# Kernel tuning notes

Measured on AMD Instinct MI355X. Metric: run time of the kernel, lower is better.

Reference implementation:

```python
import jax, jax.numpy as jnp
import numpy as np

COST_CLASS = 1.0
COST_REG = 1.0
NUM_TGT = 5  # targets per batch element, implied by `sizes = [5] * ...`

# All 5^5 = 3125 ways for each of the 5 targets to pick one of its 5 cheapest queries.
_CHOICES = np.stack(np.meshgrid(*([np.arange(NUM_TGT)] * NUM_TGT), indexing='ij'), -1).reshape(-1, NUM_TGT)


def _solve_lap5(cost):
    """Exact rectangular linear_sum_assignment for cost [num_queries, 5].

    Exchange argument: some optimal matching assigns every target (column) to one of
    its 5 cheapest queries (at most 4 of them can be taken by the other targets).
    So enumerate 5^5 candidate tuples, mask duplicates, take the argmin.
    Returns (row_ind, col_ind) sorted by row like scipy.linear_sum_assignment.
    """
    neg_vals, idx = jax.lax.top_k(-cost.T, NUM_TGT)          # [5 targets, 5 candidates]
    vals = -neg_vals
    choices = jnp.asarray(_CHOICES)                          # [3125, 5]
    t = jnp.arange(NUM_TGT)
    cand_q = idx[t[None, :], choices]                        # [3125, 5] query index per target
    cand_c = vals[t[None, :], choices]                       # [3125, 5] matching cost per target
    sq = jnp.sort(cand_q, axis=-1)
    valid = jnp.all(sq[:, 1:] != sq[:, :-1], axis=-1)        # all chosen queries distinct
    total = jnp.where(valid, cand_c.sum(-1), jnp.inf)
    best = jnp.argmin(total)
    rows = cand_q[best]                                      # [5] query index per target 0..4
    order = jnp.argsort(rows)
    return rows[order].astype(jnp.int32), order.astype(jnp.int32)


def setup_inputs() -> dict:
    key = jax.random.key(0)
    k1, k2, k3, k4 = jax.random.split(key, 4)
    bs, nq, T = 32, 2048, 32 * NUM_TGT
    return {
        'pred_logits': jax.random.normal(k1, (bs, nq, 1), dtype=jnp.float32),
        'pred_regs': jax.random.normal(k2, (bs, nq, 3), dtype=jnp.float32),
        'labels': jax.random.randint(k3, (T,), 0, 2, dtype=jnp.int32),
        'tgt_regression': jax.random.normal(k4, (T, 3), dtype=jnp.float32),
    }


def reference(pred_logits, pred_regs, labels, tgt_regression):
    bs, nq = pred_logits.shape[:2]
    # out_prob = softmax(pred_logits) is computed in the original but never used
    # (and tgt labels are unused): classification cost reduces to the constant cost_class.
    out_bbox = pred_regs.reshape(bs * nq, 3)
    # L1 cdist against ALL targets, as in the original: [bs*nq, T]
    cost_reg = jnp.sum(jnp.abs(out_bbox[:, None, :] - tgt_regression[None, :, :]), axis=-1)
    C = COST_REG * cost_reg + COST_CLASS
    # split the target axis into per-batch blocks of 5 and keep the diagonal block
    C = C.reshape(bs, nq, bs, NUM_TGT)
    b = jnp.arange(bs)
    Cb = C[b, :, b, :]                                       # [bs, nq, 5]
    rows, cols = jax.vmap(_solve_lap5)(Cb)                   # each [bs, 5]
    return rows, cols
```

## Files before the change

kernel.cpp:

```cpp
#include <hip/hip_runtime.h>

#define NUM_TGT 5

__device__ __forceinline__ bool lex_less(float c1, int q1, float c2, int q2) {
    return (c1 < c2) || (c1 == c2 && q1 < q2);
}

__device__ __forceinline__ void insert5(float c[5], int q[5], float cv, int qv) {
    if (lex_less(cv, qv, c[4], q[4])) {
        c[4] = cv; q[4] = qv;
#pragma unroll
        for (int i = 3; i >= 0; --i) {
            if (lex_less(c[i + 1], q[i + 1], c[i], q[i])) {
                float tc = c[i]; c[i] = c[i + 1]; c[i + 1] = tc;
                int   tq = q[i]; q[i] = q[i + 1]; q[i + 1] = tq;
            }
        }
    }
}

__global__ __launch_bounds__(256)
void topk_kernel(const float* __restrict__ pred_regs,
                 const float* __restrict__ tgt_reg,
                 float* __restrict__ ws_c,
                 int* __restrict__ ws_q,
                 int nq) {
    const int bt   = blockIdx.x;
    const int b    = bt / NUM_TGT;
    const int tid  = threadIdx.x;
    const int wave = tid >> 6;
    const int lane = tid & 63;

    __shared__ float wc[4][NUM_TGT];
    __shared__ int   wq[4][NUM_TGT];

    const float t0 = tgt_reg[bt * 3 + 0];
    const float t1 = tgt_reg[bt * 3 + 1];
    const float t2 = tgt_reg[bt * 3 + 2];

    float c[5] = {INFINITY, INFINITY, INFINITY, INFINITY, INFINITY};
    int   q[5] = {0x7fffffff, 0x7fffffff, 0x7fffffff, 0x7fffffff, 0x7fffffff};

    const float* base = pred_regs + (size_t)b * nq * 3;
#pragma unroll
    for (int j = 0; j < 8; ++j) {
        const int qi = j * 256 + tid;
        if (qi < nq) {
            float cost = fabsf(base[qi * 3 + 0] - t0);
            cost = cost + fabsf(base[qi * 3 + 1] - t1);
            cost = cost + fabsf(base[qi * 3 + 2] - t2);
            cost = cost + 1.0f;
            insert5(c, q, cost, qi);
        }
    }

#pragma unroll
    for (int m = 1; m < 64; m <<= 1) {
#pragma unroll
        for (int i = 0; i < 5; ++i) {
            float oc = __shfl_xor(c[i], m, 64);
            int   oq = __shfl_xor(q[i], m, 64);
            insert5(c, q, oc, oq);
        }
    }

    if (lane == 0) {
#pragma unroll
        for (int i = 0; i < 5; ++i) { wc[wave][i] = c[i]; wq[wave][i] = q[i]; }
    }
    __syncthreads();

    if (tid == 0) {
#pragma unroll
        for (int w = 1; w < 4; ++w)
#pragma unroll
            for (int i = 0; i < 5; ++i)
                insert5(c, q, wc[w][i], wq[w][i]);
#pragma unroll
        for (int i = 0; i < 5; ++i) {
            ws_c[bt * NUM_TGT + i] = c[i];
            ws_q[bt * NUM_TGT + i] = q[i];
        }
    }
}

__global__ __launch_bounds__(256)
void enumerate_kernel(const float* __restrict__ ws_c,
                      const int* __restrict__ ws_q,
                      int* __restrict__ out,
                      int bs) {
    const int b    = blockIdx.x;
    const int tid  = threadIdx.x;
    const int wave = tid >> 6;
    const int lane = tid & 63;

    __shared__ float top_c[NUM_TGT][NUM_TGT];
    __shared__ int   top_q[NUM_TGT][NUM_TGT];
    __shared__ float red_t[4];
    __shared__ int   red_k[4];

    if (tid < 25) {
        top_c[tid / 5][tid % 5] = ws_c[b * 25 + tid];
        top_q[tid / 5][tid % 5] = ws_q[b * 25 + tid];
    }
    __syncthreads();

    float bt = INFINITY;
    int   bk = 0x7fffffff;
    for (int k = tid; k < 3125; k += 256) {
        int r  = k;
        const int d0 = r / 625; r -= d0 * 625;
        const int d1 = r / 125; r -= d1 * 125;
        const int d2 = r / 25;  r -= d2 * 25;
        const int d3 = r / 5;
        const int d4 = r - d3 * 5;

        const int q0 = top_q[0][d0], q1 = top_q[1][d1], q2 = top_q[2][d2],
                  q3 = top_q[3][d3], q4 = top_q[4][d4];
        const bool valid =
            q0 != q1 && q0 != q2 && q0 != q3 && q0 != q4 &&
            q1 != q2 && q1 != q3 && q1 != q4 &&
            q2 != q3 && q2 != q4 &&
            q3 != q4;

        float tot = top_c[0][d0];
        tot = tot + top_c[1][d1];
        tot = tot + top_c[2][d2];
        tot = tot + top_c[3][d3];
        tot = tot + top_c[4][d4];
        if (!valid) tot = INFINITY;

        if (tot < bt || (tot == bt && k < bk)) { bt = tot; bk = k; }
    }

#pragma unroll
    for (int off = 32; off; off >>= 1) {
        float ot = __shfl_down(bt, off, 64);
        int   ok = __shfl_down(bk, off, 64);
        if (ot < bt || (ot == bt && ok < bk)) { bt = ot; bk = ok; }
    }
    if (lane == 0) { red_t[wave] = bt; red_k[wave] = bk; }
    __syncthreads();

    if (tid == 0) {
        float fbt = red_t[0]; int fbk = red_k[0];
#pragma unroll
        for (int w = 1; w < 4; ++w) {
            if (red_t[w] < fbt || (red_t[w] == fbt && red_k[w] < fbk)) {
                fbt = red_t[w]; fbk = red_k[w];
            }
        }
        int r = fbk;
        int d[5];
        d[0] = r / 625; r -= d[0] * 625;
        d[1] = r / 125; r -= d[1] * 125;
        d[2] = r / 25;  r -= d[2] * 25;
        d[3] = r / 5;
        d[4] = r - d[3] * 5;

        int rows[5];
#pragma unroll
        for (int t = 0; t < 5; ++t) rows[t] = top_q[t][d[t]];

#pragma unroll
        for (int i = 0; i < 5; ++i) {
            int rank = 0;
#pragma unroll
            for (int j = 0; j < 5; ++j) rank += (rows[j] < rows[i]);
            out[b * 5 + rank]          = rows[i];
            out[bs * 5 + b * 5 + rank] = i;
        }
    }
}

extern "C" void kernel_launch(void* const* d_in, const int* in_sizes, int n_in,
                              void* d_out, int out_size, void* d_ws, size_t ws_size,
                              hipStream_t stream) {
    const float* pred_regs = (const float*)d_in[1];
    const float* tgt_reg   = (const float*)d_in[3];
    int* out = (int*)d_out;

    const int T  = in_sizes[2];
    const int bs = T / NUM_TGT;
    const int nq = in_sizes[0] / bs;

    float* ws_c = (float*)d_ws;
    int*   ws_q = (int*)(ws_c + (size_t)bs * NUM_TGT * NUM_TGT);

    topk_kernel<<<bs * NUM_TGT, 256, 0, stream>>>(pred_regs, tgt_reg, ws_c, ws_q, nq);
    enumerate_kernel<<<bs, 256, 0, stream>>>(ws_c, ws_q, out, bs);
}
```

Before: 75.38 us.

## Fuse top-k and enumeration into one kernel with one wave per target

Merges the two kernels into a single launch of one block per batch element with five wavefronts. Each wavefront scans all queries for its own target, keeps a top-5 in registers, and writes it to shared memory, where the whole block then runs the 5^5 enumeration. This drops one kernel launch, the global workspace round trip and the cross-wave merge. In exchange each wave serially loops over 2048 queries (32 iterations of insert5 instead of 8), and only 32 blocks run on the GPU, so parallelism drops sharply.

New measurement: 83.15 us. +10.3%, slower.

```diff
diff --git a/kernel.cpp b/kernel.cpp
--- a/kernel.cpp
+++ b/kernel.cpp
@@ -19,21 +19,22 @@
     }
 }
 
-__global__ __launch_bounds__(256)
-void topk_kernel(const float* __restrict__ pred_regs,
-                 const float* __restrict__ tgt_reg,
-                 float* __restrict__ ws_c,
-                 int* __restrict__ ws_q,
-                 int nq) {
-    const int bt   = blockIdx.x;
-    const int b    = bt / NUM_TGT;
+__global__ __launch_bounds__(320)
+void fused_matcher_kernel(const float* __restrict__ pred_regs,
+                          const float* __restrict__ tgt_reg,
+                          int* __restrict__ out,
+                          int bs, int nq) {
+    const int b    = blockIdx.x;
     const int tid  = threadIdx.x;
     const int wave = tid >> 6;
     const int lane = tid & 63;
 
-    __shared__ float wc[4][NUM_TGT];
-    __shared__ int   wq[4][NUM_TGT];
+    __shared__ float top_c[NUM_TGT][NUM_TGT];
+    __shared__ int   top_q[NUM_TGT][NUM_TGT];
+    __shared__ float red_t[NUM_TGT];
+    __shared__ int   red_k[NUM_TGT];
 
+    const int bt = b * NUM_TGT + wave;
     const float t0 = tgt_reg[bt * 3 + 0];
     const float t1 = tgt_reg[bt * 3 + 1];
     const float t2 = tgt_reg[bt * 3 + 2];
@@ -42,16 +43,12 @@
     int   q[5] = {0x7fffffff, 0x7fffffff, 0x7fffffff, 0x7fffffff, 0x7fffffff};
 
     const float* base = pred_regs + (size_t)b * nq * 3;
-#pragma unroll
-    for (int j = 0; j < 8; ++j) {
-        const int qi = j * 256 + tid;
-        if (qi < nq) {
-            float cost = fabsf(base[qi * 3 + 0] - t0);
-            cost = cost + fabsf(base[qi * 3 + 1] - t1);
-            cost = cost + fabsf(base[qi * 3 + 2] - t2);
-            cost = cost + 1.0f;
-            insert5(c, q, cost, qi);
-        }
+    for (int qi = lane; qi < nq; qi += 64) {
+        float cost = fabsf(base[qi * 3 + 0] - t0);
+        cost = cost + fabsf(base[qi * 3 + 1] - t1);
+        cost = cost + fabsf(base[qi * 3 + 2] - t2);
+        cost = cost + 1.0f;
+        insert5(c, q, cost, qi);
     }
 
 #pragma unroll
@@ -66,48 +63,13 @@
 
     if (lane == 0) {
 #pragma unroll
-        for (int i = 0; i < 5; ++i) { wc[wave][i] = c[i]; wq[wave][i] = q[i]; }
+        for (int i = 0; i < 5; ++i) { top_c[wave][i] = c[i]; top_q[wave][i] = q[i]; }
     }
     __syncthreads();
 
-    if (tid == 0) {
-#pragma unroll
-        for (int w = 1; w < 4; ++w)
-#pragma unroll
-            for (int i = 0; i < 5; ++i)
-                insert5(c, q, wc[w][i], wq[w][i]);
-#pragma unroll
-        for (int i = 0; i < 5; ++i) {
-            ws_c[bt * NUM_TGT + i] = c[i];
-            ws_q[bt * NUM_TGT + i] = q[i];
-        }
-    }
-}
-
-__global__ __launch_bounds__(256)
-void enumerate_kernel(const float* __restrict__ ws_c,
-                      const int* __restrict__ ws_q,
-                      int* __restrict__ out,
-                      int bs) {
-    const int b    = blockIdx.x;
-    const int tid  = threadIdx.x;
-    const int wave = tid >> 6;
-    const int lane = tid & 63;
-
-    __shared__ float top_c[NUM_TGT][NUM_TGT];
-    __shared__ int   top_q[NUM_TGT][NUM_TGT];
-    __shared__ float red_t[4];
-    __shared__ int   red_k[4];
-
-    if (tid < 25) {
-        top_c[tid / 5][tid % 5] = ws_c[b * 25 + tid];
-        top_q[tid / 5][tid % 5] = ws_q[b * 25 + tid];
-    }
-    __syncthreads();
-
-    float bt = INFINITY;
-    int   bk = 0x7fffffff;
-    for (int k = tid; k < 3125; k += 256) {
+    float bcost = INFINITY;
+    int   bk    = 0x7fffffff;
+    for (int k = tid; k < 3125; k += 320) {
         int r  = k;
         const int d0 = r / 625; r -= d0 * 625;
         const int d1 = r / 125; r -= d1 * 125;
@@ -130,22 +92,22 @@
         tot = tot + top_c[4][d4];
         if (!valid) tot = INFINITY;
 
-        if (tot < bt || (tot == bt && k < bk)) { bt = tot; bk = k; }
+        if (tot < bcost || (tot == bcost && k < bk)) { bcost = tot; bk = k; }
     }
 
 #pragma unroll
     for (int off = 32; off; off >>= 1) {
-        float ot = __shfl_down(bt, off, 64);
+        float ot = __shfl_down(bcost, off, 64);
         int   ok = __shfl_down(bk, off, 64);
-        if (ot < bt || (ot == bt && ok < bk)) { bt = ot; bk = ok; }
+        if (ot < bcost || (ot == bcost && ok < bk)) { bcost = ot; bk = ok; }
     }
-    if (lane == 0) { red_t[wave] = bt; red_k[wave] = bk; }
+    if (lane == 0) { red_t[wave] = bcost; red_k[wave] = bk; }
     __syncthreads();
 
     if (tid == 0) {
         float fbt = red_t[0]; int fbk = red_k[0];
 #pragma unroll
-        for (int w = 1; w < 4; ++w) {
+        for (int w = 1; w < NUM_TGT; ++w) {
             if (red_t[w] < fbt || (red_t[w] == fbt && red_k[w] < fbk)) {
                 fbt = red_t[w]; fbk = red_k[w];
             }
@@ -184,9 +146,5 @@
     const int bs = T / NUM_TGT;
     const int nq = in_sizes[0] / bs;
 
-    float* ws_c = (float*)d_ws;
-    int*   ws_q = (int*)(ws_c + (size_t)bs * NUM_TGT * NUM_TGT);
-
-    topk_kernel<<<bs * NUM_TGT, 256, 0, stream>>>(pred_regs, tgt_reg, ws_c, ws_q, nq);
-    enumerate_kernel<<<bs, 256, 0, stream>>>(ws_c, ws_q, out, bs);
+    fused_matcher_kernel<<<bs, 64 * NUM_TGT, 0, stream>>>(pred_regs, tgt_reg, out, bs, nq);
 }
```
